# Optimization experiments

Hardware: AMD Instinct MI355X
Metric: run time of the kernel (lower is better)

## Reference

```python
import jax, jax.numpy as jnp
import numpy as np

NEG_NUM = -10000.0


def setup_inputs() -> dict:
    key = jax.random.key(0)
    ks = jax.random.split(key, 7)
    B, L, M, H, A = 32, 2048, 512, 512, 256
    memory = jax.random.normal(ks[0], (B, L, M), dtype=jnp.float32)
    hidden = jax.random.normal(ks[1], (B, H), dtype=jnp.float32)
    mask = jax.random.randint(ks[2], (B, L), 0, 2, dtype=jnp.int32)
    # ensure no fully-masked row (softmax well-defined)
    mask = mask.at[:, 0].set(1)
    # nn.Linear params: W1 (A, M+H), b1 (A,), W2 (1, A), b2 (1,)
    lim1 = 1.0 / np.sqrt(M + H)
    W1 = jax.random.uniform(ks[3], (A, M + H), jnp.float32, -lim1, lim1)
    b1 = jax.random.uniform(ks[4], (A,), jnp.float32, -lim1, lim1)
    lim2 = 1.0 / np.sqrt(A)
    W2 = jax.random.uniform(ks[5], (1, A), jnp.float32, -lim2, lim2)
    b2 = jax.random.uniform(ks[6], (1,), jnp.float32, -lim2, lim2)
    return {"memory": memory, "hidden": hidden, "mask": mask,
            "W1": W1, "b1": b1, "W2": W2, "b2": b2}


def reference(memory, hidden, mask, W1, b1, W2, b2):
    # memory: (B, L, M), hidden: (B, H)
    M = memory.shape[-1]
    # Split W1 so we never materialize the concat: equivalent to
    # Linear(cat([memory, hidden_expanded])) since cat@W1^T = mem@W1m^T + hid@W1h^T
    W1m, W1h = W1[:, :M], W1[:, M:]
    proj = (jnp.einsum('blm,am->bla', memory, W1m)
            + jnp.einsum('bh,ah->ba', hidden, W1h)[:, None, :]
            + b1)                                   # (B, L, A)
    score = jnp.einsum('bla,a->bl', jnp.tanh(proj), W2[0]) + b2[0]  # (B, L)
    score = jnp.where(mask == 0, NEG_NUM, score)
    p_memory = jax.nn.softmax(score, axis=-1)        # (B, L)
    expected_memory = jnp.einsum('bl,blm->bm', p_memory, memory)  # (B, M)
    return expected_memory, p_memory
```

## Files before the change

### kernel.cpp

```cpp
#include <hip/hip_runtime.h>
#include <hip/hip_bf16.h>

constexpr int Bb = 32;
constexpr int Ll = 2048;
constexpr int Mm = 512;
constexpr int Hh = 512;
constexpr int Aa = 256;

typedef __attribute__((ext_vector_type(4))) float f32x4;
typedef __attribute__((ext_vector_type(8))) short short8;
typedef __attribute__((ext_vector_type(4))) unsigned short ushort4v;

__device__ __forceinline__ unsigned short f2bf(float f) {
    __hip_bfloat16 h = __float2bfloat16(f);
    return *reinterpret_cast<unsigned short*>(&h);
}

__device__ __forceinline__ ushort4v cvt4(f32x4 v) {
    ushort4v o;
    o[0] = f2bf(v[0]); o[1] = f2bf(v[1]); o[2] = f2bf(v[2]); o[3] = f2bf(v[3]);
    return o;
}

__device__ __forceinline__ void gload_lds16(const void* g, void* l) {
    __builtin_amdgcn_global_load_lds(
        (const __attribute__((address_space(1))) unsigned int*)g,
        (__attribute__((address_space(3))) unsigned int*)l, 16, 0, 0);
}

__global__ void k_prep(const float* __restrict__ W1, const float* __restrict__ hidden,
                       const float* __restrict__ b1,
                       unsigned short* __restrict__ W1mb, float* __restrict__ hb) {
    const int tid = threadIdx.x;
    if (blockIdx.x < 128) {
        int i = blockIdx.x * 256 + tid;
        int a  = i >> 7;
        int mq = (i & 127) << 2;
        f32x4 v = *reinterpret_cast<const f32x4*>(W1 + (size_t)a * (Mm + Hh) + mq);
        int ks = mq >> 5;
        int kb = mq & 31;
        *reinterpret_cast<ushort4v*>(W1mb + (size_t)ks * (Aa * 32) + a * 32 + kb) = cvt4(v);
    } else {
        int b = blockIdx.x - 128;
        __shared__ float sh[Hh];
        sh[tid]       = hidden[b * Hh + tid];
        sh[tid + 256] = hidden[b * Hh + 256 + tid];
        __syncthreads();
        int a = tid;
        const float* wrow = W1 + (size_t)a * (Mm + Hh) + Mm;
        float acc = b1[a];
        #pragma unroll 8
        for (int h = 0; h < Hh; h += 4) {
            f32x4 w = *reinterpret_cast<const f32x4*>(wrow + h);
            acc += w[0] * sh[h] + w[1] * sh[h + 1] + w[2] * sh[h + 2] + w[3] * sh[h + 3];
        }
        hb[b * Aa + a] = acc;
    }
}

__launch_bounds__(256, 4)
__global__ void k_score(const float* __restrict__ mem,
                        const unsigned short* __restrict__ W1mb,
                        const float* __restrict__ hb, const float* __restrict__ W2,
                        float* __restrict__ score) {
    __shared__ unsigned short ldsA[2][64 * 32];
    __shared__ unsigned short ldsB[2][256 * 32];

    const int tid  = threadIdx.x;
    const int wave = tid >> 6;
    const int lane = tid & 63;
    const int g = lane >> 4;
    const int r = lane & 15;
    const int blockRow = blockIdx.x * 64;
    const int b = blockRow >> 11;

    f32x4 acc[16];
    #pragma unroll
    for (int ct = 0; ct < 16; ct++) acc[ct] = (f32x4){0.f, 0.f, 0.f, 0.f};

    const int c0 = tid, c1 = tid + 256;
    const float* gA0 = mem + (size_t)(blockRow + (c0 >> 3)) * Mm + (c0 & 7) * 4;
    const float* gA1 = mem + (size_t)(blockRow + (c1 >> 3)) * Mm + (c1 & 7) * 4;
    const char* gB = (const char*)W1mb;

    {
        #pragma unroll
        for (int j = 0; j < 4; ++j)
            gload_lds16(gB + (size_t)(wave * 4 + j) * 1024 + lane * 16,
                        &ldsB[0][(wave * 4 + j) * 512]);
        f32x4 a0 = *reinterpret_cast<const f32x4*>(gA0);
        f32x4 a1 = *reinterpret_cast<const f32x4*>(gA1);
        *reinterpret_cast<ushort4v*>(&ldsA[0][c0 * 4]) = cvt4(a0);
        *reinterpret_cast<ushort4v*>(&ldsA[0][c1 * 4]) = cvt4(a1);
    }
    f32x4 p0 = *reinterpret_cast<const f32x4*>(gA0 + 32);
    f32x4 p1 = *reinterpret_cast<const f32x4*>(gA1 + 32);
    __syncthreads();

    for (int ks = 0; ks < 16; ++ks) {
        const int cur = ks & 1, nxt = cur ^ 1;
        if (ks < 15) {
            #pragma unroll
            for (int j = 0; j < 4; ++j)
                gload_lds16(gB + (size_t)(ks + 1) * 16384 + (wave * 4 + j) * 1024 + lane * 16,
                            &ldsB[nxt][(wave * 4 + j) * 512]);
            *reinterpret_cast<ushort4v*>(&ldsA[nxt][c0 * 4]) = cvt4(p0);
            *reinterpret_cast<ushort4v*>(&ldsA[nxt][c1 * 4]) = cvt4(p1);
        }
        if (ks < 14) {
            p0 = *reinterpret_cast<const f32x4*>(gA0 + (ks + 2) * 32);
            p1 = *reinterpret_cast<const f32x4*>(gA1 + (ks + 2) * 32);
        }
        short8 af = *reinterpret_cast<const short8*>(&ldsA[cur][(wave * 16 + r) * 32 + g * 8]);
        #pragma unroll
        for (int h = 0; h < 4; ++h) {
            short8 bf[4];
            #pragma unroll
            for (int j = 0; j < 4; ++j)
                bf[j] = *reinterpret_cast<const short8*>(&ldsB[cur][((h * 4 + j) * 16 + r) * 32 + g * 8]);
            #pragma unroll
            for (int j = 0; j < 4; ++j)
                acc[h * 4 + j] = __builtin_amdgcn_mfma_f32_16x16x32_bf16(af, bf[j], acc[h * 4 + j], 0, 0, 0);
        }
        __syncthreads();
    }

    float s[4] = {0.f, 0.f, 0.f, 0.f};
    #pragma unroll
    for (int ct = 0; ct < 16; ++ct) {
        int a = ct * 16 + r;
        float hba = hb[b * Aa + a];
        float w2a = W2[a];
        #pragma unroll
        for (int reg = 0; reg < 4; ++reg) {
            float pr = acc[ct][reg] + hba;
            float e = __expf(2.f * pr);
            float t = (e - 1.f) * __builtin_amdgcn_rcpf(e + 1.f);
            s[reg] += t * w2a;
        }
    }
    #pragma unroll
    for (int off = 1; off < 16; off <<= 1) {
        #pragma unroll
        for (int reg = 0; reg < 4; ++reg) s[reg] += __shfl_xor(s[reg], off, 64);
    }
    if (r == 0) {
        #pragma unroll
        for (int reg = 0; reg < 4; ++reg)
            score[blockRow + wave * 16 + g * 4 + reg] = s[reg];
    }
}

__launch_bounds__(256)
__global__ void k_exp1(const float* __restrict__ mem, const float* __restrict__ score,
                       const int* __restrict__ mask,
                       float* __restrict__ p, float* __restrict__ partial) {
    const int b   = blockIdx.x >> 6;
    const int lc  = blockIdx.x & 63;
    const int tid = threadIdx.x;
    const int wave = tid >> 6;
    __shared__ float redmx[4];
    __shared__ float redsm[4];
    __shared__ float sp[32];
    __shared__ f32x4 sacc[128];

    const float* sb = score + b * Ll;
    const int*   mb = mask + b * Ll;

    float v[8]; int mk[8];
    #pragma unroll
    for (int i = 0; i < 8; i++) {
        int l = i * 256 + tid;
        v[i]  = sb[l];
        mk[i] = mb[l];
    }
    float mx = -1e30f;
    #pragma unroll
    for (int i = 0; i < 8; i++) if (mk[i]) mx = fmaxf(mx, v[i]);
    #pragma unroll
    for (int off = 1; off < 64; off <<= 1) mx = fmaxf(mx, __shfl_xor(mx, off, 64));
    if ((tid & 63) == 0) redmx[wave] = mx;
    __syncthreads();
    mx = fmaxf(fmaxf(redmx[0], redmx[1]), fmaxf(redmx[2], redmx[3]));

    float s = 0.f;
    #pragma unroll
    for (int i = 0; i < 8; i++) s += mk[i] ? __expf(v[i] - mx) : 0.f;
    #pragma unroll
    for (int off = 1; off < 64; off <<= 1) s += __shfl_xor(s, off, 64);
    if ((tid & 63) == 0) redsm[wave] = s;
    __syncthreads();
    s = redsm[0] + redsm[1] + redsm[2] + redsm[3];
    const float inv = 1.f / s;

    if (tid < 32) {
        int l = lc * 32 + tid;
        float pv = mb[l] ? __expf(sb[l] - mx) * inv : 0.f;
        sp[tid] = pv;
        p[b * Ll + l] = pv;
    }
    __syncthreads();

    const int half = tid >> 7, cq = tid & 127;
    const float* base = mem + ((size_t)b * Ll + lc * 32) * Mm + cq * 4;
    f32x4 acc = (f32x4){0.f, 0.f, 0.f, 0.f};
    for (int rr = half; rr < 32; rr += 2)
        acc += sp[rr] * *reinterpret_cast<const f32x4*>(base + (size_t)rr * Mm);
    if (half == 1) sacc[cq] = acc;
    __syncthreads();
    if (half == 0) {
        acc += sacc[cq];
        *reinterpret_cast<f32x4*>(partial + (size_t)blockIdx.x * Mm + cq * 4) = acc;
    }
}

__global__ void k_exp2(const float* __restrict__ partial, float* __restrict__ out) {
    const int b  = blockIdx.x;
    const int mi = threadIdx.x;
    const float* pb = partial + (size_t)b * 64 * Mm + mi * 4;
    f32x4 acc = (f32x4){0.f, 0.f, 0.f, 0.f};
    #pragma unroll 8
    for (int c = 0; c < 64; ++c)
        acc += *reinterpret_cast<const f32x4*>(pb + (size_t)c * Mm);
    *reinterpret_cast<f32x4*>(out + b * Mm + mi * 4) = acc;
}

extern "C" void kernel_launch(void* const* d_in, const int* in_sizes, int n_in,
                              void* d_out, int out_size, void* d_ws, size_t ws_size,
                              hipStream_t stream) {
    const float* memory = (const float*)d_in[0];
    const float* hidden = (const float*)d_in[1];
    const int*   mask   = (const int*)d_in[2];
    const float* W1     = (const float*)d_in[3];
    const float* b1     = (const float*)d_in[4];
    const float* W2     = (const float*)d_in[5];
    float* out = (float*)d_out;

    unsigned short* W1mb = (unsigned short*)d_ws;
    float* hb      = (float*)((char*)d_ws + 256 * 1024);
    float* score   = (float*)((char*)d_ws + 288 * 1024);
    float* partial = (float*)((char*)d_ws + 1024 * 1024);
    float* p = out + Bb * Mm;

    k_prep<<<160, 256, 0, stream>>>(W1, hidden, b1, W1mb, hb);
    k_score<<<1024, 256, 0, stream>>>(memory, W1mb, hb, W2, score);
    k_exp1<<<2048, 256, 0, stream>>>(memory, score, mask, p, partial);
    k_exp2<<<32, 128, 0, stream>>>(partial, out);
}
```

Measured before the change: 256.6 us.

## Switch score GEMM to 32x32 MFMA tiles with swizzled LDS layout

The score kernel moves from 16x16x32 MFMA, where each wave covered 16 rows by all 256 columns, to 32x32x16 MFMA, where each wave covers all 64 rows by 64 columns. The epilogue now reduces across waves through LDS. An XOR swizzle is added to both the A tile and the prepacked W1 layout to avoid LDS bank conflicts, and fewer LDS fragment reads are needed per MFMA. The expectation kernel now handles 64 rows per block with half as many blocks and partials, which cuts redundant softmax reductions. In exchange it adds an extra barrier and cross-wave reduction, and each block has less parallelism.

```diff
diff --git a/kernel.cpp b/kernel.cpp
--- a/kernel.cpp
+++ b/kernel.cpp
@@ -8,6 +8,7 @@
 constexpr int Aa = 256;
 
 typedef __attribute__((ext_vector_type(4))) float f32x4;
+typedef __attribute__((ext_vector_type(16))) float f32x16;
 typedef __attribute__((ext_vector_type(8))) short short8;
 typedef __attribute__((ext_vector_type(4))) unsigned short ushort4v;
 
@@ -39,7 +40,8 @@
         f32x4 v = *reinterpret_cast<const f32x4*>(W1 + (size_t)a * (Mm + Hh) + mq);
         int ks = mq >> 5;
         int kb = mq & 31;
-        *reinterpret_cast<ushort4v*>(W1mb + (size_t)ks * (Aa * 32) + a * 32 + kb) = cvt4(v);
+        int kswz = kb ^ ((a & 3) << 3);
+        *reinterpret_cast<ushort4v*>(W1mb + (size_t)ks * (Aa * 32) + a * 32 + kswz) = cvt4(v);
     } else {
         int b = blockIdx.x - 128;
         __shared__ float sh[Hh];
@@ -69,29 +71,45 @@
     const int tid  = threadIdx.x;
     const int wave = tid >> 6;
     const int lane = tid & 63;
-    const int g = lane >> 4;
-    const int r = lane & 15;
+    const int l31  = lane & 31;
+    const int hi   = lane >> 5;
     const int blockRow = blockIdx.x * 64;
     const int b = blockRow >> 11;
 
-    f32x4 acc[16];
-    #pragma unroll
-    for (int ct = 0; ct < 16; ct++) acc[ct] = (f32x4){0.f, 0.f, 0.f, 0.f};
+    f32x16 acc[2][2];
+    #pragma unroll
+    for (int i = 0; i < 2; i++)
+        #pragma unroll
+        for (int j = 0; j < 2; j++)
+            #pragma unroll
+            for (int e = 0; e < 16; e++) acc[i][j][e] = 0.f;
 
     const int c0 = tid, c1 = tid + 256;
-    const float* gA0 = mem + (size_t)(blockRow + (c0 >> 3)) * Mm + (c0 & 7) * 4;
-    const float* gA1 = mem + (size_t)(blockRow + (c1 >> 3)) * Mm + (c1 & 7) * 4;
+    const int ar0 = c0 >> 3, ak0 = (c0 & 7) * 4;
+    const int ar1 = c1 >> 3, ak1 = (c1 & 7) * 4;
+    const int sa0 = ar0 * 32 + (ak0 ^ ((ar0 & 3) << 3));
+    const int sa1 = ar1 * 32 + (ak1 ^ ((ar1 & 3) << 3));
+    const float* gA0 = mem + (size_t)(blockRow + ar0) * Mm + ak0;
+    const float* gA1 = mem + (size_t)(blockRow + ar1) * Mm + ak1;
     const char* gB = (const char*)W1mb;
 
+    const int swz = (l31 & 3) << 3;
+    const int aoff0 = (hi * 8) ^ swz;
+    const int aoff1 = (hi * 8 + 16) ^ swz;
+    const int arow0 = l31 * 32;
+    const int arow1 = (32 + l31) * 32;
+    const int brow0 = (wave * 64 + l31) * 32;
+    const int brow1 = (wave * 64 + 32 + l31) * 32;
+
+    #pragma unroll
+    for (int j = 0; j < 4; ++j)
+        gload_lds16(gB + (size_t)(wave * 4 + j) * 1024 + lane * 16,
+                    &ldsB[0][(wave * 4 + j) * 512]);
     {
-        #pragma unroll
-        for (int j = 0; j < 4; ++j)
-            gload_lds16(gB + (size_t)(wave * 4 + j) * 1024 + lane * 16,
-                        &ldsB[0][(wave * 4 + j) * 512]);
         f32x4 a0 = *reinterpret_cast<const f32x4*>(gA0);
         f32x4 a1 = *reinterpret_cast<const f32x4*>(gA1);
-        *reinterpret_cast<ushort4v*>(&ldsA[0][c0 * 4]) = cvt4(a0);
-        *reinterpret_cast<ushort4v*>(&ldsA[0][c1 * 4]) = cvt4(a1);
+        *reinterpret_cast<ushort4v*>(&ldsA[0][sa0]) = cvt4(a0);
+        *reinterpret_cast<ushort4v*>(&ldsA[0][sa1]) = cvt4(a1);
     }
     f32x4 p0 = *reinterpret_cast<const f32x4*>(gA0 + 32);
     f32x4 p1 = *reinterpret_cast<const f32x4*>(gA1 + 32);
@@ -104,64 +122,84 @@
             for (int j = 0; j < 4; ++j)
                 gload_lds16(gB + (size_t)(ks + 1) * 16384 + (wave * 4 + j) * 1024 + lane * 16,
                             &ldsB[nxt][(wave * 4 + j) * 512]);
-            *reinterpret_cast<ushort4v*>(&ldsA[nxt][c0 * 4]) = cvt4(p0);
-            *reinterpret_cast<ushort4v*>(&ldsA[nxt][c1 * 4]) = cvt4(p1);
+            *reinterpret_cast<ushort4v*>(&ldsA[nxt][sa0]) = cvt4(p0);
+            *reinterpret_cast<ushort4v*>(&ldsA[nxt][sa1]) = cvt4(p1);
         }
         if (ks < 14) {
             p0 = *reinterpret_cast<const f32x4*>(gA0 + (ks + 2) * 32);
             p1 = *reinterpret_cast<const f32x4*>(gA1 + (ks + 2) * 32);
         }
-        short8 af = *reinterpret_cast<const short8*>(&ldsA[cur][(wave * 16 + r) * 32 + g * 8]);
-        #pragma unroll
-        for (int h = 0; h < 4; ++h) {
-            short8 bf[4];
-            #pragma unroll
-            for (int j = 0; j < 4; ++j)
-                bf[j] = *reinterpret_cast<const short8*>(&ldsB[cur][((h * 4 + j) * 16 + r) * 32 + g * 8]);
-            #pragma unroll
-            for (int j = 0; j < 4; ++j)
-                acc[h * 4 + j] = __builtin_amdgcn_mfma_f32_16x16x32_bf16(af, bf[j], acc[h * 4 + j], 0, 0, 0);
+        const unsigned short* A  = ldsA[cur];
+        const unsigned short* Bt = ldsB[cur];
+        #pragma unroll
+        for (int kk = 0; kk < 2; ++kk) {
+            const int ao = kk ? aoff1 : aoff0;
+            short8 a0 = *reinterpret_cast<const short8*>(&A[arow0 + ao]);
+            short8 a1 = *reinterpret_cast<const short8*>(&A[arow1 + ao]);
+            short8 b0 = *reinterpret_cast<const short8*>(&Bt[brow0 + ao]);
+            short8 b1 = *reinterpret_cast<const short8*>(&Bt[brow1 + ao]);
+            acc[0][0] = __builtin_amdgcn_mfma_f32_32x32x16_bf16(a0, b0, acc[0][0], 0, 0, 0);
+            acc[0][1] = __builtin_amdgcn_mfma_f32_32x32x16_bf16(a0, b1, acc[0][1], 0, 0, 0);
+            acc[1][0] = __builtin_amdgcn_mfma_f32_32x32x16_bf16(a1, b0, acc[1][0], 0, 0, 0);
+            acc[1][1] = __builtin_amdgcn_mfma_f32_32x32x16_bf16(a1, b1, acc[1][1], 0, 0, 0);
         }
         __syncthreads();
     }
 
-    float s[4] = {0.f, 0.f, 0.f, 0.f};
-    #pragma unroll
-    for (int ct = 0; ct < 16; ++ct) {
-        int a = ct * 16 + r;
+    float sc[2][16];
+    #pragma unroll
+    for (int tr = 0; tr < 2; tr++)
+        #pragma unroll
+        for (int rg = 0; rg < 16; rg++) sc[tr][rg] = 0.f;
+    #pragma unroll
+    for (int tc = 0; tc < 2; ++tc) {
+        int a = wave * 64 + tc * 32 + l31;
         float hba = hb[b * Aa + a];
         float w2a = W2[a];
         #pragma unroll
-        for (int reg = 0; reg < 4; ++reg) {
-            float pr = acc[ct][reg] + hba;
-            float e = __expf(2.f * pr);
-            float t = (e - 1.f) * __builtin_amdgcn_rcpf(e + 1.f);
-            s[reg] += t * w2a;
-        }
-    }
-    #pragma unroll
-    for (int off = 1; off < 16; off <<= 1) {
-        #pragma unroll
-        for (int reg = 0; reg < 4; ++reg) s[reg] += __shfl_xor(s[reg], off, 64);
-    }
-    if (r == 0) {
-        #pragma unroll
-        for (int reg = 0; reg < 4; ++reg)
-            score[blockRow + wave * 16 + g * 4 + reg] = s[reg];
-    }
+        for (int tr = 0; tr < 2; tr++)
+            #pragma unroll
+            for (int rg = 0; rg < 16; rg++) {
+                float pr = acc[tr][tc][rg] + hba;
+                float e = __expf(2.f * pr);
+                float t = (e - 1.f) * __builtin_amdgcn_rcpf(e + 1.f);
+                sc[tr][rg] += t * w2a;
+            }
+    }
+    #pragma unroll
+    for (int off = 1; off < 32; off <<= 1)
+        #pragma unroll
+        for (int tr = 0; tr < 2; tr++)
+            #pragma unroll
+            for (int rg = 0; rg < 16; rg++)
+                sc[tr][rg] += __shfl_xor(sc[tr][rg], off, 64);
+    float* sred = (float*)&ldsA[0][0];
+    if (l31 == 0) {
+        #pragma unroll
+        for (int tr = 0; tr < 2; tr++)
+            #pragma unroll
+            for (int rg = 0; rg < 16; rg++) {
+                int row = tr * 32 + (rg & 3) + 8 * (rg >> 2) + 4 * hi;
+                sred[row * 4 + wave] = sc[tr][rg];
+            }
+    }
+    __syncthreads();
+    if (tid < 64)
+        score[blockRow + tid] = sred[tid * 4] + sred[tid * 4 + 1]
+                              + sred[tid * 4 + 2] + sred[tid * 4 + 3];
 }
 
 __launch_bounds__(256)
 __global__ void k_exp1(const float* __restrict__ mem, const float* __restrict__ score,
                        const int* __restrict__ mask,
                        float* __restrict__ p, float* __restrict__ partial) {
-    const int b   = blockIdx.x >> 6;
-    const int lc  = blockIdx.x & 63;
+    const int b   = blockIdx.x >> 5;
+    const int lc  = blockIdx.x & 31;
     const int tid = threadIdx.x;
     const int wave = tid >> 6;
     __shared__ float redmx[4];
     __shared__ float redsm[4];
-    __shared__ float sp[32];
+    __shared__ float sp[64];
     __shared__ f32x4 sacc[128];
 
     const float* sb = score + b * Ll;
@@ -193,8 +231,8 @@
     s = redsm[0] + redsm[1] + redsm[2] + redsm[3];
     const float inv = 1.f / s;
 
-    if (tid < 32) {
-        int l = lc * 32 + tid;
+    if (tid < 64) {
+        int l = lc * 64 + tid;
         float pv = mb[l] ? __expf(sb[l] - mx) * inv : 0.f;
         sp[tid] = pv;
         p[b * Ll + l] = pv;
@@ -202,9 +240,10 @@
     __syncthreads();
 
     const int half = tid >> 7, cq = tid & 127;
-    const float* base = mem + ((size_t)b * Ll + lc * 32) * Mm + cq * 4;
+    const float* base = mem + ((size_t)b * Ll + lc * 64) * Mm + cq * 4;
     f32x4 acc = (f32x4){0.f, 0.f, 0.f, 0.f};
-    for (int rr = half; rr < 32; rr += 2)
+    #pragma unroll 8
+    for (int rr = half; rr < 64; rr += 2)
         acc += sp[rr] * *reinterpret_cast<const f32x4*>(base + (size_t)rr * Mm);
     if (half == 1) sacc[cq] = acc;
     __syncthreads();
@@ -217,10 +256,10 @@
 __global__ void k_exp2(const float* __restrict__ partial, float* __restrict__ out) {
     const int b  = blockIdx.x;
     const int mi = threadIdx.x;
-    const float* pb = partial + (size_t)b * 64 * Mm + mi * 4;
+    const float* pb = partial + (size_t)b * 32 * Mm + mi * 4;
     f32x4 acc = (f32x4){0.f, 0.f, 0.f, 0.f};
     #pragma unroll 8
-    for (int c = 0; c < 64; ++c)
+    for (int c = 0; c < 32; ++c)
         acc += *reinterpret_cast<const f32x4*>(pb + (size_t)c * Mm);
     *reinterpret_cast<f32x4*>(out + b * Mm + mi * 4) = acc;
 }
@@ -244,6 +283,6 @@
 
     k_prep<<<160, 256, 0, stream>>>(W1, hidden, b1, W1mb, hb);
     k_score<<<1024, 256, 0, stream>>>(memory, W1mb, hb, W2, score);
-    k_exp1<<<2048, 256, 0, stream>>>(memory, score, mask, p, partial);
+    k_exp1<<<1024, 256, 0, stream>>>(memory, score, mask, p, partial);
     k_exp2<<<32, 128, 0, stream>>>(partial, out);
 }
```

Measured after the change: 254.1 us. About the same (-1.0%).
